# Kernel tuning notes

Measured on AMD Instinct MI355X. Metric: run time of the kernel, lower is better.

## Reference

```python
import jax, jax.numpy as jnp
import numpy as np

# Mamba2 config fixed by the wrapper: state=32, expand=1, n_groups=1, conv kernel=4
H, P, N, K = 32, 64, 32, 4          # heads, head_dim, state_size, conv kernel
D_MODEL = H * P                      # hidden = intermediate (expand=1) = 2048
CONV_DIM = D_MODEL + 2 * N           # intermediate + 2*n_groups*state = 2112
PROJ = D_MODEL + CONV_DIM + H        # in_proj width = 4192
EPS = 1e-6


def setup_inputs() -> dict:
    key = jax.random.key(0)
    ks = jax.random.split(key, 8)
    B, L = 4, 2048
    w = lambda k, shape, sc=0.02: jax.random.normal(k, shape, jnp.float32) * sc
    return {
        "x": jax.random.normal(ks[0], (B, L, D_MODEL), jnp.float32),
        "W_in": w(ks[1], (D_MODEL, PROJ)),
        "b_in": jnp.zeros((PROJ,), jnp.float32),
        "conv_w": w(ks[2], (CONV_DIM, K), 0.25),
        "conv_b": jnp.zeros((CONV_DIM,), jnp.float32),
        "A_log": jnp.log(jnp.arange(1, H + 1, dtype=jnp.float32)),
        "dt_bias": jax.random.uniform(ks[3], (H,), jnp.float32, -4.0, 0.0),
        "D_param": jnp.ones((H,), jnp.float32),
        "norm_w": jnp.ones((D_MODEL,), jnp.float32),
        "W_out": w(ks[4], (D_MODEL, D_MODEL)),
    }


def reference(x, W_in, b_in, conv_w, conv_b, A_log, dt_bias, D_param, norm_w, W_out):
    B, L, _ = x.shape
    proj = x @ W_in + b_in                                   # (B,L,PROJ)
    gate, hBC, dt_raw = jnp.split(proj, [D_MODEL, D_MODEL + CONV_DIM], axis=-1)

    # causal depthwise conv1d over time (kernel K, left pad K-1), then SiLU
    hp = jnp.pad(hBC, ((0, 0), (K - 1, 0), (0, 0)))
    conv = conv_b + sum(hp[:, k:k + L, :] * conv_w[:, k] for k in range(K))
    conv = jax.nn.silu(conv)

    xs, Bm, Cm = jnp.split(conv, [D_MODEL, D_MODEL + N], axis=-1)
    xs = xs.reshape(B, L, H, P)                              # (B,L,H,P)

    A = -jnp.exp(A_log)                                      # (H,)
    dt = jax.nn.softplus(dt_raw + dt_bias)                   # (B,L,H)
    dA = jnp.exp(dt * A)                                     # (B,L,H)

    def step(hstate, inp):
        dA_t, dt_t, x_t, B_t, C_t = inp                      # (B,H),(B,H),(B,H,P),(B,N),(B,N)
        upd = (dt_t[:, :, None] * x_t)[..., None] * B_t[:, None, None, :]
        hstate = dA_t[:, :, None, None] * hstate + upd       # (B,H,P,N)
        y_t = jnp.einsum('bhpn,bn->bhp', hstate, C_t)
        return hstate, y_t

    h0 = jnp.zeros((B, H, P, N), x.dtype)
    scan_in = (dA.transpose(1, 0, 2), dt.transpose(1, 0, 2),
               xs.transpose(1, 0, 2, 3), Bm.transpose(1, 0, 2), Cm.transpose(1, 0, 2))
    _, ys = jax.lax.scan(step, h0, scan_in)                  # ys: (L,B,H,P)

    y = ys.transpose(1, 0, 2, 3) + D_param[None, None, :, None] * xs
    y = y.reshape(B, L, D_MODEL)

    # gated RMSNorm: gate applied before normalization (MambaRMSNormGated)
    y = y * jax.nn.silu(gate)
    var = jnp.mean(jnp.square(y), axis=-1, keepdims=True)
    y = y * jax.lax.rsqrt(var + EPS) * norm_w
    return y @ W_out
```

## Files before the change

### kernel.cpp

```cpp
#include <hip/hip_runtime.h>
#include <cstdint>
#include <cstddef>

constexpr int kB    = 4;
constexpr int kL    = 2048;
constexpr int kH    = 32;
constexpr int kP    = 64;
constexpr int kN    = 32;
constexpr int kD    = 2048;
constexpr int kProjW = 4192;
constexpr int kLdp  = 4224;
constexpr int kM    = kB * kL;
constexpr int kK    = kD;
constexpr int kLC   = 64;
constexpr int kNC   = kL / kLC;

typedef _Float16 f16x8 __attribute__((ext_vector_type(8)));
typedef float f32x4 __attribute__((ext_vector_type(4)));

__device__ __forceinline__ float lane_bcast(float v, int lane) {
    return __int_as_float(__builtin_amdgcn_readlane(__float_as_int(v), lane));
}
__device__ __forceinline__ float silu_f(float x) { return x / (1.f + __expf(-x)); }

__device__ __forceinline__ void async_copy16(const void* g, void* lds) {
    __builtin_amdgcn_global_load_lds(
        (const __attribute__((address_space(1))) unsigned int*)(uintptr_t)g,
        (__attribute__((address_space(3))) unsigned int*)(uintptr_t)lds,
        16, 0, 0);
}

__global__ __launch_bounds__(256) void cast_f16_kernel(const float* __restrict__ in,
                                                       _Float16* __restrict__ out) {
    size_t i = ((size_t)blockIdx.x * 256 + threadIdx.x) * 8;
    float4 a = *(const float4*)(in + i);
    float4 b = *(const float4*)(in + i + 4);
    f16x8 o;
    o[0] = (_Float16)a.x; o[1] = (_Float16)a.y; o[2] = (_Float16)a.z; o[3] = (_Float16)a.w;
    o[4] = (_Float16)b.x; o[5] = (_Float16)b.y; o[6] = (_Float16)b.z; o[7] = (_Float16)b.w;
    *(f16x8*)(out + i) = o;
}

__global__ __launch_bounds__(256) void transpose_cast_kernel(const float* __restrict__ W,
                                                             _Float16* __restrict__ Wt,
                                                             int R, int C) {
    __shared__ float tile[32][33];
    const int c0 = blockIdx.x * 32;
    const int r0 = blockIdx.y * 32;
    const int tx = threadIdx.x & 31;
    const int ty = threadIdx.x >> 5;
    #pragma unroll
    for (int i = 0; i < 32; i += 8) {
        int rr = r0 + ty + i;
        int cc = c0 + tx;
        tile[ty + i][tx] = (cc < C) ? W[(size_t)rr * C + cc] : 0.f;
    }
    __syncthreads();
    #pragma unroll
    for (int i = 0; i < 32; i += 8) {
        int cc = c0 + ty + i;
        int rr = r0 + tx;
        Wt[(size_t)cc * R + rr] = (_Float16)tile[tx][ty + i];
    }
}

template <bool OUT_F16>
__global__ __launch_bounds__(512, 2) void gemm256_kernel(
    const _Float16* __restrict__ A, const _Float16* __restrict__ Bt,
    const float* __restrict__ bias, int nbias,
    void* __restrict__ Cout, int K, int ldc, int nvalid, int nn)
{
    __shared__ __attribute__((aligned(16))) _Float16 lds[2 * 4 * 8192];

    const int tid = threadIdx.x;
    const int l = tid & 63, r = l & 15, q = l >> 4;
    const int w = tid >> 6, wm = w >> 2, wn = w & 3;

    const int nwg = gridDim.x;
    const int q8 = nwg >> 3;
    const int pid = blockIdx.x;
    const int wg = (pid & 7) * q8 + (pid >> 3);
    const int m_idx = wg / nn;
    const int n_idx = wg - m_idx * nn;
    const size_t tileM = (size_t)m_idx * 256;
    const size_t tileN = (size_t)n_idx * 256;

    const int sR = ((tid >> 7) << 4) | (tid & 15);
    const int sC = ((tid >> 4) & 7) << 3;
    const _Float16* aSrc = A  + (tileM + sR) * (size_t)K + sC;
    const _Float16* bSrc = Bt + (tileN + sR) * (size_t)K + sC;
    _Float16* dst0 = lds + tid * 8;

    auto STAGE = [&](int buf, int part, const _Float16* src, int half, int kt2) {
        const _Float16* s = src + (size_t)(half * 128) * K + kt2 * 64;
        _Float16* d = dst0 + buf * 32768 + part * 8192;
        async_copy16(s, d);
        async_copy16(s + (size_t)64 * K, d + 4096);
    };

    const int NT = K >> 5 >> 1;
    STAGE(0, 0, aSrc, 0, 0); STAGE(0, 1, aSrc, 1, 0);
    STAGE(0, 2, bSrc, 0, 0); STAGE(0, 3, bSrc, 1, 0);
    STAGE(1, 0, aSrc, 0, 1); STAGE(1, 3, bSrc, 1, 1);
    asm volatile("s_waitcnt vmcnt(4)" ::: "memory");
    asm volatile("s_barrier" ::: "memory");

    f32x4 acc[8][4] = {};
    f16x8 afr[4][2], bfr[2][2], bfr2[2][2];

    const int aRd = wm * 4 * 2048 + l * 16;
    const int bRd = wn * 2 * 2048 + l * 16;

#define MFMA_CL(AO, BO, BARR, KK)                                                        \
    _Pragma("unroll")                                                                    \
    for (int i = 0; i < 4; ++i)                                                          \
        _Pragma("unroll")                                                                \
        for (int j = 0; j < 2; ++j)                                                      \
            acc[(AO) + i][(BO) + j] = __builtin_amdgcn_mfma_f32_16x16x32_f16(            \
                afr[i][KK], BARR[j][KK], acc[(AO) + i][(BO) + j], 0, 0, 0);

    for (int kt = 0; kt < NT; ++kt) {
        const int bsel = kt & 1;
        const char* a0p = (const char*)lds + bsel * 65536;
        const char* a1p = a0p + 16384;
        const char* b0p = a0p + 2 * 16384;
        const char* b1p = a0p + 3 * 16384;

        afr[0][0] = *(const f16x8*)(a0p + aRd);
        afr[1][0] = *(const f16x8*)(a0p + aRd + 2048);
        afr[2][0] = *(const f16x8*)(a0p + aRd + 4096);
        afr[3][0] = *(const f16x8*)(a0p + aRd + 6144);
        afr[0][1] = *(const f16x8*)(a0p + aRd + 1024);
        afr[1][1] = *(const f16x8*)(a0p + aRd + 3072);
        afr[2][1] = *(const f16x8*)(a0p + aRd + 5120);
        afr[3][1] = *(const f16x8*)(a0p + aRd + 7168);
        bfr[0][0] = *(const f16x8*)(b0p + bRd);
        bfr[1][0] = *(const f16x8*)(b0p + bRd + 2048);
        bfr[0][1] = *(const f16x8*)(b0p + bRd + 1024);
        bfr[1][1] = *(const f16x8*)(b0p + bRd + 3072);
        __builtin_amdgcn_sched_barrier(0);
        bfr2[0][0] = *(const f16x8*)(b1p + bRd);
        bfr2[1][0] = *(const f16x8*)(b1p + bRd + 2048);
        bfr2[0][1] = *(const f16x8*)(b1p + bRd + 1024);
        bfr2[1][1] = *(const f16x8*)(b1p + bRd + 3072);
        if (kt + 1 < NT) {
            STAGE(bsel ^ 1, 2, bSrc, 0, kt + 1);
            STAGE(bsel ^ 1, 1, aSrc, 1, kt + 1);
        }
        asm volatile("s_waitcnt lgkmcnt(4)" ::: "memory");
        __builtin_amdgcn_sched_barrier(0);
        __builtin_amdgcn_s_setprio(1);
        MFMA_CL(0, 0, bfr, 0)
        MFMA_CL(0, 0, bfr, 1)
        asm volatile("s_waitcnt lgkmcnt(0)" ::: "memory");
        __builtin_amdgcn_sched_barrier(0);
        MFMA_CL(0, 2, bfr2, 0)
        MFMA_CL(0, 2, bfr2, 1)
        __builtin_amdgcn_s_setprio(0);

        afr[0][0] = *(const f16x8*)(a1p + aRd);
        afr[1][0] = *(const f16x8*)(a1p + aRd + 2048);
        afr[2][0] = *(const f16x8*)(a1p + aRd + 4096);
        afr[3][0] = *(const f16x8*)(a1p + aRd + 6144);
        afr[0][1] = *(const f16x8*)(a1p + aRd + 1024);
        afr[1][1] = *(const f16x8*)(a1p + aRd + 3072);
        afr[2][1] = *(const f16x8*)(a1p + aRd + 5120);
        afr[3][1] = *(const f16x8*)(a1p + aRd + 7168);
        asm volatile("s_barrier" ::: "memory");
        if (kt + 2 < NT) {
            STAGE(bsel, 0, aSrc, 0, kt + 2);
            STAGE(bsel, 3, bSrc, 1, kt + 2);
        }
        asm volatile("s_waitcnt lgkmcnt(0)" ::: "memory");
        __builtin_amdgcn_sched_barrier(0);
        __builtin_amdgcn_s_setprio(1);
        MFMA_CL(4, 2, bfr2, 0)
        MFMA_CL(4, 2, bfr2, 1)
        MFMA_CL(4, 0, bfr, 0)
        MFMA_CL(4, 0, bfr, 1)
        __builtin_amdgcn_s_setprio(0);
        if (kt + 2 < NT) asm volatile("s_waitcnt vmcnt(4)" ::: "memory");
        else             asm volatile("s_waitcnt vmcnt(0)" ::: "memory");
        asm volatile("s_barrier" ::: "memory");
    }
#undef MFMA_CL

    #pragma unroll
    for (int bb = 0; bb < 4; ++bb) {
        const int nh = bb >> 1, j = bb & 1;
        const int col = (int)tileN + nh * 128 + wn * 32 + j * 16 + r;
        if (col >= nvalid) continue;
        float bv = 0.f;
        if (bias != nullptr && col < nbias) bv = bias[col];
        #pragma unroll
        for (int aa = 0; aa < 8; ++aa) {
            const int mh = aa >> 2, i = aa & 3;
            const size_t row = tileM + (size_t)(mh * 128 + wm * 64 + i * 16 + q * 4);
            #pragma unroll
            for (int u = 0; u < 4; ++u) {
                float v = acc[aa][bb][u] + bv;
                if (OUT_F16) ((_Float16*)Cout)[(row + u) * (size_t)ldc + col] = (_Float16)v;
                else         ((float*)Cout)[(row + u) * (size_t)ldc + col] = v;
            }
        }
    }
}

__global__ __launch_bounds__(256) void gemm_tail_kernel(
    const _Float16* __restrict__ A, const _Float16* __restrict__ Bt,
    const float* __restrict__ bias , _Float16* __restrict__ Cout,
    const float* __restrict__ A_log, const float* __restrict__ dt_bias,
    float* __restrict__ dtv, float* __restrict__ dAv)
{
    __shared__ __attribute__((aligned(16))) _Float16 lds[2 * 10240];
    const int K = kK;
    const int tid = threadIdx.x;
    const int l = tid & 63, r = l & 15, q = l >> 4;
    const int w = tid >> 6;
    const size_t tileM = (size_t)blockIdx.x * 32;

    const int sRa = ((tid >> 7) << 4) | (tid & 15);
    const int sC  = ((tid >> 4) & 7) << 3;
    const _Float16* aSrc = A + (tileM + sRa) * (size_t)K + sC;
    const _Float16* bSrc = Bt + (size_t)sRa * K + sC;
    _Float16* dst0 = lds + tid * 8;

    auto STG = [&](int buf, int kt2) {
        const _Float16* a = aSrc + kt2 * 64;
        const _Float16* b = bSrc + kt2 * 64;
        _Float16* d = dst0 + buf * 10240;
        async_copy16(a, d);
        #pragma unroll
        for (int c = 0; c < 4; ++c)
            async_copy16(b + (size_t)(c * 32) * K, d + 2048 + c * 2048);
    };

    const int NT = K / 64;
    STG(0, 0); STG(1, 1);
    asm volatile("s_waitcnt vmcnt(5)" ::: "memory");
    asm volatile("s_barrier" ::: "memory");

    f32x4 acc[2][2] = {};
    f16x8 af[2][2], bf[2][2];
    const int aRdT = l * 16;
    const int bRdT = 4096 + w * 2 * 2048 + l * 16;

    for (int kt = 0; kt < NT; ++kt) {
        const char* base = (const char*)lds + (kt & 1) * 20480;
        af[0][0] = *(const f16x8*)(base + aRdT);
        af[1][0] = *(const f16x8*)(base + aRdT + 2048);
        af[0][1] = *(const f16x8*)(base + aRdT + 1024);
        af[1][1] = *(const f16x8*)(base + aRdT + 3072);
        bf[0][0] = *(const f16x8*)(base + bRdT);
        bf[1][0] = *(const f16x8*)(base + bRdT + 2048);
        bf[0][1] = *(const f16x8*)(base + bRdT + 1024);
        bf[1][1] = *(const f16x8*)(base + bRdT + 3072);
        asm volatile("s_waitcnt lgkmcnt(0)" ::: "memory");
        __builtin_amdgcn_sched_barrier(0);
        asm volatile("s_barrier" ::: "memory");
        if (kt + 2 < NT) STG(kt & 1, kt + 2);
        #pragma unroll
        for (int kk = 0; kk < 2; ++kk)
            #pragma unroll
            for (int i = 0; i < 2; ++i)
                #pragma unroll
                for (int j = 0; j < 2; ++j)
                    acc[i][j] = __builtin_amdgcn_mfma_f32_16x16x32_f16(af[i][kk], bf[j][kk], acc[i][j], 0, 0, 0);
        if (kt + 2 < NT) asm volatile("s_waitcnt vmcnt(5)" ::: "memory");
        else             asm volatile("s_waitcnt vmcnt(0)" ::: "memory");
        asm volatile("s_barrier" ::: "memory");
    }

    #pragma unroll
    for (int j = 0; j < 2; ++j) {
        const int colOff = w * 32 + j * 16 + r;
        const float bv = (colOff < 96) ? bias[colOff] : 0.f;
        #pragma unroll
        for (int i = 0; i < 2; ++i) {
            #pragma unroll
            for (int u = 0; u < 4; ++u) {
                const size_t row = tileM + (size_t)(i * 16 + q * 4 + u);
                float v = acc[i][j][u] + bv;
                Cout[row * kLdp + 4096 + colOff] = (_Float16)v;
            }
        }
        if (colOff >= 64 && colOff < 96) {
            const int h = colOff - 64;
            const float db = dt_bias[h];
            const float nA = -expf(A_log[h]);
            #pragma unroll
            for (int i = 0; i < 2; ++i) {
                #pragma unroll
                for (int u = 0; u < 4; ++u) {
                    const size_t row = tileM + (size_t)(i * 16 + q * 4 + u);
                    const int b = (int)(row >> 11), t = (int)(row & 2047);
                    float z = acc[i][j][u] + bv + db;
                    float dt = (z > 20.f) ? z : log1pf(expf(z));
                    float dA = expf(dt * nA);
                    const size_t idx = (((size_t)b * kH + h) << 11) | t;
                    dtv[idx] = dt;
                    dAv[idx] = dA;
                }
            }
        }
    }
}

__global__ __launch_bounds__(64) void scan_pass1_kernel(
    const _Float16* __restrict__ projh, const float* __restrict__ conv_w,
    const float* __restrict__ conv_b, const float* __restrict__ dtv,
    const float* __restrict__ dAv, float* __restrict__ cstate, float* __restrict__ Pch)
{
    const int blk = blockIdx.x;
    const int c   = blk & (kNC - 1);
    const int bh  = blk >> 5;
    const int h   = bh & (kH - 1);
    const int b   = bh >> 5;
    const int l   = threadIdx.x;
    const int t0  = c * kLC;

    const int chx = h * kP + l;
    const int chb = 2048 + (l & 31);
    const float xw0 = conv_w[chx*4+0], xw1 = conv_w[chx*4+1], xw2 = conv_w[chx*4+2], xw3 = conv_w[chx*4+3];
    const float xbb = conv_b[chx];
    const float bw0 = conv_w[chb*4+0], bw1 = conv_w[chb*4+1], bw2 = conv_w[chb*4+2], bw3 = conv_w[chb*4+3];
    const float bbb = conv_b[chb];

    const _Float16* pb = projh + (size_t)b * kL * kLdp;
    const int colx = 2048 + chx;
    const int colb = 2048 + chb;

    float xq0=0.f, xq1=0.f, xq2=0.f, bq0=0.f, bq1=0.f, bq2=0.f;
    if (c > 0) {
        xq0 = (float)pb[(size_t)(t0-3)*kLdp + colx];
        xq1 = (float)pb[(size_t)(t0-2)*kLdp + colx];
        xq2 = (float)pb[(size_t)(t0-1)*kLdp + colx];
        bq0 = (float)pb[(size_t)(t0-3)*kLdp + colb];
        bq1 = (float)pb[(size_t)(t0-2)*kLdp + colb];
        bq2 = (float)pb[(size_t)(t0-1)*kLdp + colb];
    }

    float hs[kN];
    #pragma unroll
    for (int n = 0; n < kN; ++n) hs[n] = 0.f;
    float Pp = 1.f;
    const float* dtp = dtv + (size_t)bh * kL;
    const float* dAp = dAv + (size_t)bh * kL;

    float xv = (float)pb[(size_t)t0 * kLdp + colx];
    float bv = (float)pb[(size_t)t0 * kLdp + colb];
    float dt = dtp[t0], dA = dAp[t0];

    #pragma unroll 1
    for (int t = t0; t < t0 + kLC; ++t) {
        float xn = 0.f, bn = 0.f, dtn = 0.f, dAn = 0.f;
        if (t + 1 < t0 + kLC) {
            const size_t ro2 = (size_t)(t + 1) * kLdp;
            xn = (float)pb[ro2 + colx];
            bn = (float)pb[ro2 + colb];
            dtn = dtp[t + 1]; dAn = dAp[t + 1];
        }
        float sx = silu_f(xbb + xw0*xq0 + xw1*xq1 + xw2*xq2 + xw3*xv);
        float sb = silu_f(bbb + bw0*bq0 + bw1*bq1 + bw2*bq2 + bw3*bv);
        xq0=xq1; xq1=xq2; xq2=xv;
        bq0=bq1; bq1=bq2; bq2=bv;
        float dtx = dt * sx;
        Pp *= dA;
        #pragma unroll
        for (int n = 0; n < kN; ++n)
            hs[n] = fmaf(dA, hs[n], dtx * lane_bcast(sb, n));
        xv = xn; bv = bn; dt = dtn; dA = dAn;
    }
    float* cs = cstate + (size_t)blk * (kP * kN) + l * kN;
    #pragma unroll
    for (int n = 0; n < kN; ++n) cs[n] = hs[n];
    if (l == 0) Pch[blk] = Pp;
}

__global__ __launch_bounds__(256) void scan_pass2_kernel(float* __restrict__ cstate,
                                                         const float* __restrict__ Pch) {
    const int bh  = blockIdx.x;
    const int off = threadIdx.x * 8;
    float s[8];
    #pragma unroll
    for (int i = 0; i < 8; ++i) s[i] = 0.f;
    float* base = cstate + (size_t)bh * (kNC * kP * kN) + off;
    #pragma unroll 1
    for (int c = 0; c < kNC; ++c) {
        float* cs = base + c * (kP * kN);
        float Pp = Pch[bh * kNC + c];
        #pragma unroll
        for (int i = 0; i < 8; ++i) {
            float loc = cs[i];
            cs[i] = s[i];
            s[i] = fmaf(Pp, s[i], loc);
        }
    }
}

__global__ __launch_bounds__(64) void scan_pass3_kernel(
    const _Float16* __restrict__ projh, const float* __restrict__ conv_w,
    const float* __restrict__ conv_b, const float* __restrict__ dtv,
    const float* __restrict__ dAv, const float* __restrict__ cstate,
    const float* __restrict__ D_param, float* __restrict__ ypre)
{
    const int blk = blockIdx.x;
    const int c   = blk & (kNC - 1);
    const int bh  = blk >> 5;
    const int h   = bh & (kH - 1);
    const int b   = bh >> 5;
    const int l   = threadIdx.x;
    const int t0  = c * kLC;

    const int chx = h * kP + l;
    const int chc = 2048 + l;
    const float xw0 = conv_w[chx*4+0], xw1 = conv_w[chx*4+1], xw2 = conv_w[chx*4+2], xw3 = conv_w[chx*4+3];
    const float xbb = conv_b[chx];
    const float cw0 = conv_w[chc*4+0], cw1 = conv_w[chc*4+1], cw2 = conv_w[chc*4+2], cw3 = conv_w[chc*4+3];
    const float cbb = conv_b[chc];

    const _Float16* pb = projh + (size_t)b * kL * kLdp;
    const int colx = 2048 + chx;
    const int colc = 2048 + chc;

    float xq0=0.f, xq1=0.f, xq2=0.f, cq0=0.f, cq1=0.f, cq2=0.f;
    if (c > 0) {
        xq0 = (float)pb[(size_t)(t0-3)*kLdp + colx];
        xq1 = (float)pb[(size_t)(t0-2)*kLdp + colx];
        xq2 = (float)pb[(size_t)(t0-1)*kLdp + colx];
        cq0 = (float)pb[(size_t)(t0-3)*kLdp + colc];
        cq1 = (float)pb[(size_t)(t0-2)*kLdp + colc];
        cq2 = (float)pb[(size_t)(t0-1)*kLdp + colc];
    }

    float hs[kN];
    const float* cs = cstate + (size_t)blk * (kP * kN) + l * kN;
    #pragma unroll
    for (int n = 0; n < kN; ++n) hs[n] = cs[n];
    const float Dh = D_param[h];
    const float* dtp = dtv + (size_t)bh * kL;
    const float* dAp = dAv + (size_t)bh * kL;
    float* yo = ypre + (size_t)b * kL * kD + h * kP + l;

    float xv = (float)pb[(size_t)t0 * kLdp + colx];
    float cv = (float)pb[(size_t)t0 * kLdp + colc];
    float dt = dtp[t0], dA = dAp[t0];

    #pragma unroll 1
    for (int t = t0; t < t0 + kLC; ++t) {
        float xn = 0.f, cn2 = 0.f, dtn = 0.f, dAn = 0.f;
        if (t + 1 < t0 + kLC) {
            const size_t ro2 = (size_t)(t + 1) * kLdp;
            xn = (float)pb[ro2 + colx];
            cn2 = (float)pb[ro2 + colc];
            dtn = dtp[t + 1]; dAn = dAp[t + 1];
        }
        float sx = silu_f(xbb + xw0*xq0 + xw1*xq1 + xw2*xq2 + xw3*xv);
        float sc = silu_f(cbb + cw0*cq0 + cw1*cq1 + cw2*cq2 + cw3*cv);
        xq0=xq1; xq1=xq2; xq2=xv;
        cq0=cq1; cq1=cq2; cq2=cv;
        float dtx = dt * sx;
        float y0 = Dh * sx, y1 = 0.f;
        #pragma unroll
        for (int n = 0; n < kN; ++n) {
            float bn = lane_bcast(sc, n);
            float cn = lane_bcast(sc, n + 32);
            hs[n] = fmaf(dA, hs[n], dtx * bn);
            if (n & 1) y1 = fmaf(hs[n], cn, y1);
            else       y0 = fmaf(hs[n], cn, y0);
        }
        yo[(size_t)t * kD] = y0 + y1;
        xv = xn; cv = cn2; dt = dtn; dA = dAn;
    }
}

__global__ __launch_bounds__(256) void gated_norm_kernel(
    const float* __restrict__ ypre, const _Float16* __restrict__ projh,
    const float* __restrict__ norm_w, _Float16* __restrict__ yh)
{
    const int row = blockIdx.x;
    const int tid = threadIdx.x;
    const float* yr = ypre + (size_t)row * kD;
    const _Float16* gr = projh + (size_t)row * kLdp;
    float v[8];
    float ss = 0.f;
    #pragma unroll
    for (int u = 0; u < 8; ++u) {
        int col = tid + u * 256;
        float g = (float)gr[col];
        float t = yr[col] * (g / (1.f + __expf(-g)));
        v[u] = t;
        ss = fmaf(t, t, ss);
    }
    #pragma unroll
    for (int off = 32; off > 0; off >>= 1) ss += __shfl_xor(ss, off, 64);
    __shared__ float red[4];
    if ((tid & 63) == 0) red[tid >> 6] = ss;
    __syncthreads();
    float tot = (red[0] + red[1]) + (red[2] + red[3]);
    float scl = rsqrtf(tot * (1.f / (float)kD) + 1e-6f);
    #pragma unroll
    for (int u = 0; u < 8; ++u) {
        int col = tid + u * 256;
        yh[(size_t)row * kD + col] = (_Float16)(v[u] * scl * norm_w[col]);
    }
}

extern "C" void kernel_launch(void* const* d_in, const int* in_sizes, int n_in,
                              void* d_out, int out_size, void* d_ws, size_t ws_size,
                              hipStream_t stream)
{
    (void)in_sizes; (void)n_in; (void)out_size; (void)ws_size;
    const float* x       = (const float*)d_in[0];
    const float* W_in    = (const float*)d_in[1];
    const float* b_in    = (const float*)d_in[2];
    const float* conv_w  = (const float*)d_in[3];
    const float* conv_b  = (const float*)d_in[4];
    const float* A_log   = (const float*)d_in[5];
    const float* dt_bias = (const float*)d_in[6];
    const float* D_param = (const float*)d_in[7];
    const float* norm_w  = (const float*)d_in[8];
    const float* W_out   = (const float*)d_in[9];
    float* out = (float*)d_out;

    char* p = (char*)d_ws;
    _Float16* projh = (_Float16*)p; p += (size_t)kM * kLdp * 2;
    _Float16* xh    = (_Float16*)p; p += (size_t)kM * kD * 2;
    _Float16* Wt    = (_Float16*)p; p += (size_t)kLdp * kK * 2;
    _Float16* Wot   = (_Float16*)p; p += (size_t)kD * kK * 2;
    float* dtv      = (float*)p;    p += (size_t)kB * kH * kL * 4;
    float* dAv      = (float*)p;    p += (size_t)kB * kH * kL * 4;
    float* Pch      = (float*)p;    p += (size_t)kB * kH * kNC * 4;
    float* cstate = (float*)xh;
    _Float16* yh  = xh;
    float* ypre = out;

    cast_f16_kernel<<<(kM * kD) / (256 * 8), 256, 0, stream>>>(x, xh);
    transpose_cast_kernel<<<dim3(kLdp / 32, kK / 32), 256, 0, stream>>>(W_in, Wt, kK, kProjW);
    transpose_cast_kernel<<<dim3(kD / 32, kK / 32), 256, 0, stream>>>(W_out, Wot, kK, kD);
    gemm256_kernel<true><<<512, 512, 0, stream>>>(
        xh, Wt, b_in, kProjW, (void*)projh, kK, kLdp, 4096, 16);
    gemm_tail_kernel<<<kM / 32, 256, 0, stream>>>(
        xh, Wt + (size_t)4096 * kK, b_in + 4096, projh, A_log, dt_bias, dtv, dAv);
    scan_pass1_kernel<<<kB * kH * kNC, 64, 0, stream>>>(projh, conv_w, conv_b, dtv, dAv, cstate, Pch);
    scan_pass2_kernel<<<kB * kH, 256, 0, stream>>>(cstate, Pch);
    scan_pass3_kernel<<<kB * kH * kNC, 64, 0, stream>>>(projh, conv_w, conv_b, dtv, dAv, cstate, D_param, ypre);
    gated_norm_kernel<<<kM, 256, 0, stream>>>(ypre, projh, norm_w, yh);
    gemm256_kernel<false><<<256, 512, 0, stream>>>(
        yh, Wot, nullptr, 0, (void*)out, kK, kD, kD, 8);
}
```

Baseline: 620.2 us.

## Simplify GEMM double-buffer pipeline and stagger LDS quadrant order across wave groups

Replaces the split half-tile prefetch (two stages issued at different points with a mid-iteration barrier) with a plain double buffer that prefetches the whole next K-tile at loop top and waits vmcnt(0) once per iteration. Odd wave groups read the A/B quadrants in the opposite order from even groups, which is meant to spread LDS bank and port pressure and drops the intra-iteration barrier. The cost is less overlap between global loads and compute, because each iteration now waits for all outstanding loads before it can continue.

```diff
diff --git a/kernel.cpp b/kernel.cpp
--- a/kernel.cpp
+++ b/kernel.cpp
@@ -98,11 +98,10 @@
         async_copy16(s + (size_t)64 * K, d + 4096);
     };
 
-    const int NT = K >> 5 >> 1;
+    const int NT = K >> 6;
     STAGE(0, 0, aSrc, 0, 0); STAGE(0, 1, aSrc, 1, 0);
     STAGE(0, 2, bSrc, 0, 0); STAGE(0, 3, bSrc, 1, 0);
-    STAGE(1, 0, aSrc, 0, 1); STAGE(1, 3, bSrc, 1, 1);
-    asm volatile("s_waitcnt vmcnt(4)" ::: "memory");
+    asm volatile("s_waitcnt vmcnt(0)" ::: "memory");
     asm volatile("s_barrier" ::: "memory");
 
     f32x4 acc[8][4] = {};
@@ -119,71 +118,90 @@
             acc[(AO) + i][(BO) + j] = __builtin_amdgcn_mfma_f32_16x16x32_f16(            \
                 afr[i][KK], BARR[j][KK], acc[(AO) + i][(BO) + j], 0, 0, 0);
 
-    for (int kt = 0; kt < NT; ++kt) {
-        const int bsel = kt & 1;
-        const char* a0p = (const char*)lds + bsel * 65536;
-        const char* a1p = a0p + 16384;
-        const char* b0p = a0p + 2 * 16384;
-        const char* b1p = a0p + 3 * 16384;
-
-        afr[0][0] = *(const f16x8*)(a0p + aRd);
-        afr[1][0] = *(const f16x8*)(a0p + aRd + 2048);
-        afr[2][0] = *(const f16x8*)(a0p + aRd + 4096);
-        afr[3][0] = *(const f16x8*)(a0p + aRd + 6144);
-        afr[0][1] = *(const f16x8*)(a0p + aRd + 1024);
-        afr[1][1] = *(const f16x8*)(a0p + aRd + 3072);
-        afr[2][1] = *(const f16x8*)(a0p + aRd + 5120);
-        afr[3][1] = *(const f16x8*)(a0p + aRd + 7168);
-        bfr[0][0] = *(const f16x8*)(b0p + bRd);
-        bfr[1][0] = *(const f16x8*)(b0p + bRd + 2048);
-        bfr[0][1] = *(const f16x8*)(b0p + bRd + 1024);
-        bfr[1][1] = *(const f16x8*)(b0p + bRd + 3072);
-        __builtin_amdgcn_sched_barrier(0);
-        bfr2[0][0] = *(const f16x8*)(b1p + bRd);
-        bfr2[1][0] = *(const f16x8*)(b1p + bRd + 2048);
-        bfr2[0][1] = *(const f16x8*)(b1p + bRd + 1024);
-        bfr2[1][1] = *(const f16x8*)(b1p + bRd + 3072);
-        if (kt + 1 < NT) {
-            STAGE(bsel ^ 1, 2, bSrc, 0, kt + 1);
-            STAGE(bsel ^ 1, 1, aSrc, 1, kt + 1);
-        }
-        asm volatile("s_waitcnt lgkmcnt(4)" ::: "memory");
-        __builtin_amdgcn_sched_barrier(0);
-        __builtin_amdgcn_s_setprio(1);
-        MFMA_CL(0, 0, bfr, 0)
-        MFMA_CL(0, 0, bfr, 1)
-        asm volatile("s_waitcnt lgkmcnt(0)" ::: "memory");
-        __builtin_amdgcn_sched_barrier(0);
-        MFMA_CL(0, 2, bfr2, 0)
-        MFMA_CL(0, 2, bfr2, 1)
-        __builtin_amdgcn_s_setprio(0);
-
-        afr[0][0] = *(const f16x8*)(a1p + aRd);
-        afr[1][0] = *(const f16x8*)(a1p + aRd + 2048);
-        afr[2][0] = *(const f16x8*)(a1p + aRd + 4096);
-        afr[3][0] = *(const f16x8*)(a1p + aRd + 6144);
-        afr[0][1] = *(const f16x8*)(a1p + aRd + 1024);
-        afr[1][1] = *(const f16x8*)(a1p + aRd + 3072);
-        afr[2][1] = *(const f16x8*)(a1p + aRd + 5120);
-        afr[3][1] = *(const f16x8*)(a1p + aRd + 7168);
-        asm volatile("s_barrier" ::: "memory");
-        if (kt + 2 < NT) {
-            STAGE(bsel, 0, aSrc, 0, kt + 2);
-            STAGE(bsel, 3, bSrc, 1, kt + 2);
-        }
-        asm volatile("s_waitcnt lgkmcnt(0)" ::: "memory");
-        __builtin_amdgcn_sched_barrier(0);
-        __builtin_amdgcn_s_setprio(1);
-        MFMA_CL(4, 2, bfr2, 0)
-        MFMA_CL(4, 2, bfr2, 1)
-        MFMA_CL(4, 0, bfr, 0)
-        MFMA_CL(4, 0, bfr, 1)
-        __builtin_amdgcn_s_setprio(0);
-        if (kt + 2 < NT) asm volatile("s_waitcnt vmcnt(4)" ::: "memory");
-        else             asm volatile("s_waitcnt vmcnt(0)" ::: "memory");
-        asm volatile("s_barrier" ::: "memory");
+#define RD_A(PBASE)                                                                      \
+    afr[0][0] = *(const f16x8*)((PBASE) + aRd);                                          \
+    afr[1][0] = *(const f16x8*)((PBASE) + aRd + 2048);                                   \
+    afr[2][0] = *(const f16x8*)((PBASE) + aRd + 4096);                                   \
+    afr[3][0] = *(const f16x8*)((PBASE) + aRd + 6144);                                   \
+    afr[0][1] = *(const f16x8*)((PBASE) + aRd + 1024);                                   \
+    afr[1][1] = *(const f16x8*)((PBASE) + aRd + 3072);                                   \
+    afr[2][1] = *(const f16x8*)((PBASE) + aRd + 5120);                                   \
+    afr[3][1] = *(const f16x8*)((PBASE) + aRd + 7168);
+
+#define RD_B(DST, PBASE)                                                                 \
+    DST[0][0] = *(const f16x8*)((PBASE) + bRd);                                          \
+    DST[1][0] = *(const f16x8*)((PBASE) + bRd + 2048);                                   \
+    DST[0][1] = *(const f16x8*)((PBASE) + bRd + 1024);                                   \
+    DST[1][1] = *(const f16x8*)((PBASE) + bRd + 3072);
+
+#define TILE_BODY(PAF, PBF, PBS, PAS, AOF, BOF, AOS, BOS)                                \
+    RD_A(PAF)                                                                            \
+    RD_B(bfr, PBF)                                                                       \
+    __builtin_amdgcn_sched_barrier(0);                                                   \
+    RD_B(bfr2, PBS)                                                                      \
+    __builtin_amdgcn_sched_barrier(0);                                                   \
+    asm volatile("s_waitcnt lgkmcnt(4)" ::: "memory");                                   \
+    __builtin_amdgcn_sched_barrier(0);                                                   \
+    __builtin_amdgcn_s_setprio(1);                                                       \
+    MFMA_CL(AOF, BOF, bfr, 0)                                                            \
+    MFMA_CL(AOF, BOF, bfr, 1)                                                            \
+    asm volatile("s_waitcnt lgkmcnt(0)" ::: "memory");                                   \
+    __builtin_amdgcn_sched_barrier(0);                                                   \
+    MFMA_CL(AOF, BOS, bfr2, 0)                                                           \
+    MFMA_CL(AOF, BOS, bfr2, 1)                                                           \
+    __builtin_amdgcn_s_setprio(0);                                                       \
+    RD_A(PAS)                                                                            \
+    __builtin_amdgcn_sched_barrier(0);                                                   \
+    asm volatile("s_waitcnt lgkmcnt(0)" ::: "memory");                                   \
+    __builtin_amdgcn_sched_barrier(0);                                                   \
+    __builtin_amdgcn_s_setprio(1);                                                       \
+    MFMA_CL(AOS, BOS, bfr2, 0)                                                           \
+    MFMA_CL(AOS, BOS, bfr2, 1)                                                           \
+    MFMA_CL(AOS, BOF, bfr, 0)                                                            \
+    MFMA_CL(AOS, BOF, bfr, 1)                                                            \
+    __builtin_amdgcn_s_setprio(0);
+
+#define TILE_STAGE_AND_SYNC                                                              \
+    if (kt + 1 < NT) {                                                                   \
+        STAGE(bsel ^ 1, 0, aSrc, 0, kt + 1);                                             \
+        STAGE(bsel ^ 1, 1, aSrc, 1, kt + 1);                                             \
+        STAGE(bsel ^ 1, 2, bSrc, 0, kt + 1);                                             \
+        STAGE(bsel ^ 1, 3, bSrc, 1, kt + 1);                                             \
+    }
+
+    const bool oddgrp = ((w >> 2) & 1) != 0;
+    if (!oddgrp) {
+        #pragma unroll 2
+        for (int kt = 0; kt < NT; ++kt) {
+            const int bsel = kt & 1;
+            const char* a0p = (const char*)lds + bsel * 65536;
+            const char* a1p = a0p + 16384;
+            const char* b0p = a0p + 2 * 16384;
+            const char* b1p = a0p + 3 * 16384;
+            TILE_STAGE_AND_SYNC
+            TILE_BODY(a0p, b0p, b1p, a1p, 0, 0, 4, 2)
+            asm volatile("s_waitcnt vmcnt(0)" ::: "memory");
+            asm volatile("s_barrier" ::: "memory");
+        }
+    } else {
+        #pragma unroll 2
+        for (int kt = 0; kt < NT; ++kt) {
+            const int bsel = kt & 1;
+            const char* a0p = (const char*)lds + bsel * 65536;
+            const char* a1p = a0p + 16384;
+            const char* b0p = a0p + 2 * 16384;
+            const char* b1p = a0p + 3 * 16384;
+            TILE_STAGE_AND_SYNC
+            TILE_BODY(a1p, b1p, b0p, a0p, 4, 2, 0, 0)
+            asm volatile("s_waitcnt vmcnt(0)" ::: "memory");
+            asm volatile("s_barrier" ::: "memory");
+        }
     }
 #undef MFMA_CL
+#undef RD_A
+#undef RD_B
+#undef TILE_BODY
+#undef TILE_STAGE_AND_SYNC
 
     #pragma unroll
     for (int bb = 0; bb < 4; ++bb) {
```

After: 649.3 us. +4.7%, slower.

## Replace 256x256 GEMM with 128x256 tile, 3-stage LDS pipeline

Applied to the files above, without the earlier changes.

Rewrites the main GEMM kernel to use 128x256 output tiles per 256-thread workgroup with a k-step of 32 and a triple-buffered LDS ring in place of the 256x256, 512-thread, double-buffered layout with split A/B halves. Each wave now computes a 64x128 sub-tile with one set of fragment loads per iteration, and both GEMM launches double their grid size. The aim is more workgroups for better CU occupancy and deeper prefetch. The cost is lower arithmetic intensity per tile, more global and LDS traffic, and a loop schedule that interleaves LDS reads with MFMA less finely. The nbias/nvalid guards are removed.

```diff
diff --git a/kernel.cpp b/kernel.cpp
--- a/kernel.cpp
+++ b/kernel.cpp
@@ -65,16 +65,16 @@
 }
 
 template <bool OUT_F16>
-__global__ __launch_bounds__(512, 2) void gemm256_kernel(
+__global__ __launch_bounds__(256, 2) void gemm128_kernel(
     const _Float16* __restrict__ A, const _Float16* __restrict__ Bt,
-    const float* __restrict__ bias, int nbias,
-    void* __restrict__ Cout, int K, int ldc, int nvalid, int nn)
+    const float* __restrict__ bias,
+    void* __restrict__ Cout, int K, int ldc, int nn)
 {
-    __shared__ __attribute__((aligned(16))) _Float16 lds[2 * 4 * 8192];
+    __shared__ __attribute__((aligned(16))) _Float16 lds[3 * 12288];
 
     const int tid = threadIdx.x;
     const int l = tid & 63, r = l & 15, q = l >> 4;
-    const int w = tid >> 6, wm = w >> 2, wn = w & 3;
+    const int w = tid >> 6, wm = w >> 1, wn = w & 1;
 
     const int nwg = gridDim.x;
     const int q8 = nwg >> 3;
@@ -82,123 +82,76 @@
     const int wg = (pid & 7) * q8 + (pid >> 3);
     const int m_idx = wg / nn;
     const int n_idx = wg - m_idx * nn;
-    const size_t tileM = (size_t)m_idx * 256;
+    const size_t tileM = (size_t)m_idx * 128;
     const size_t tileN = (size_t)n_idx * 256;
 
-    const int sR = ((tid >> 7) << 4) | (tid & 15);
-    const int sC = ((tid >> 4) & 7) << 3;
+    const int sR = ((tid >> 6) << 4) | (tid & 15);
+    const int sC = ((tid >> 4) & 3) << 3;
     const _Float16* aSrc = A  + (tileM + sR) * (size_t)K + sC;
     const _Float16* bSrc = Bt + (tileN + sR) * (size_t)K + sC;
     _Float16* dst0 = lds + tid * 8;
 
-    auto STAGE = [&](int buf, int part, const _Float16* src, int half, int kt2) {
-        const _Float16* s = src + (size_t)(half * 128) * K + kt2 * 64;
-        _Float16* d = dst0 + buf * 32768 + part * 8192;
-        async_copy16(s, d);
-        async_copy16(s + (size_t)64 * K, d + 4096);
+    auto STAGE = [&](int buf, int kt2) {
+        const _Float16* a = aSrc + kt2 * 32;
+        const _Float16* b = bSrc + kt2 * 32;
+        _Float16* d = dst0 + buf * 12288;
+        async_copy16(a, d);
+        async_copy16(a + (size_t)64 * K, d + 2048);
+        #pragma unroll
+        for (int c = 0; c < 4; ++c)
+            async_copy16(b + (size_t)(c * 64) * K, d + 4096 + c * 2048);
     };
 
-    const int NT = K >> 5 >> 1;
-    STAGE(0, 0, aSrc, 0, 0); STAGE(0, 1, aSrc, 1, 0);
-    STAGE(0, 2, bSrc, 0, 0); STAGE(0, 3, bSrc, 1, 0);
-    STAGE(1, 0, aSrc, 0, 1); STAGE(1, 3, bSrc, 1, 1);
-    asm volatile("s_waitcnt vmcnt(4)" ::: "memory");
+    const int NT = K >> 5;
+    STAGE(0, 0); STAGE(1, 1);
+    asm volatile("s_waitcnt vmcnt(6)" ::: "memory");
     asm volatile("s_barrier" ::: "memory");
 
-    f32x4 acc[8][4] = {};
-    f16x8 afr[4][2], bfr[2][2], bfr2[2][2];
-
-    const int aRd = wm * 4 * 2048 + l * 16;
-    const int bRd = wn * 2 * 2048 + l * 16;
-
-#define MFMA_CL(AO, BO, BARR, KK)                                                        \
-    _Pragma("unroll")                                                                    \
-    for (int i = 0; i < 4; ++i)                                                          \
-        _Pragma("unroll")                                                                \
-        for (int j = 0; j < 2; ++j)                                                      \
-            acc[(AO) + i][(BO) + j] = __builtin_amdgcn_mfma_f32_16x16x32_f16(            \
-                afr[i][KK], BARR[j][KK], acc[(AO) + i][(BO) + j], 0, 0, 0);
-
+    f32x4 acc[4][8] = {};
+    f16x8 af[4], bf[8];
+
+    const int aRd = wm * 4096 + l * 16;
+    const int bRd = 8192 + wn * 8192 + l * 16;
+
+    int cs = 0;
     for (int kt = 0; kt < NT; ++kt) {
-        const int bsel = kt & 1;
-        const char* a0p = (const char*)lds + bsel * 65536;
-        const char* a1p = a0p + 16384;
-        const char* b0p = a0p + 2 * 16384;
-        const char* b1p = a0p + 3 * 16384;
-
-        afr[0][0] = *(const f16x8*)(a0p + aRd);
-        afr[1][0] = *(const f16x8*)(a0p + aRd + 2048);
-        afr[2][0] = *(const f16x8*)(a0p + aRd + 4096);
-        afr[3][0] = *(const f16x8*)(a0p + aRd + 6144);
-        afr[0][1] = *(const f16x8*)(a0p + aRd + 1024);
-        afr[1][1] = *(const f16x8*)(a0p + aRd + 3072);
-        afr[2][1] = *(const f16x8*)(a0p + aRd + 5120);
-        afr[3][1] = *(const f16x8*)(a0p + aRd + 7168);
-        bfr[0][0] = *(const f16x8*)(b0p + bRd);
-        bfr[1][0] = *(const f16x8*)(b0p + bRd + 2048);
-        bfr[0][1] = *(const f16x8*)(b0p + bRd + 1024);
-        bfr[1][1] = *(const f16x8*)(b0p + bRd + 3072);
-        __builtin_amdgcn_sched_barrier(0);
-        bfr2[0][0] = *(const f16x8*)(b1p + bRd);
-        bfr2[1][0] = *(const f16x8*)(b1p + bRd + 2048);
-        bfr2[0][1] = *(const f16x8*)(b1p + bRd + 1024);
-        bfr2[1][1] = *(const f16x8*)(b1p + bRd + 3072);
-        if (kt + 1 < NT) {
-            STAGE(bsel ^ 1, 2, bSrc, 0, kt + 1);
-            STAGE(bsel ^ 1, 1, aSrc, 1, kt + 1);
-        }
-        asm volatile("s_waitcnt lgkmcnt(4)" ::: "memory");
-        __builtin_amdgcn_sched_barrier(0);
-        __builtin_amdgcn_s_setprio(1);
-        MFMA_CL(0, 0, bfr, 0)
-        MFMA_CL(0, 0, bfr, 1)
-        asm volatile("s_waitcnt lgkmcnt(0)" ::: "memory");
-        __builtin_amdgcn_sched_barrier(0);
-        MFMA_CL(0, 2, bfr2, 0)
-        MFMA_CL(0, 2, bfr2, 1)
-        __builtin_amdgcn_s_setprio(0);
-
-        afr[0][0] = *(const f16x8*)(a1p + aRd);
-        afr[1][0] = *(const f16x8*)(a1p + aRd + 2048);
-        afr[2][0] = *(const f16x8*)(a1p + aRd + 4096);
-        afr[3][0] = *(const f16x8*)(a1p + aRd + 6144);
-        afr[0][1] = *(const f16x8*)(a1p + aRd + 1024);
-        afr[1][1] = *(const f16x8*)(a1p + aRd + 3072);
-        afr[2][1] = *(const f16x8*)(a1p + aRd + 5120);
-        afr[3][1] = *(const f16x8*)(a1p + aRd + 7168);
-        asm volatile("s_barrier" ::: "memory");
+        const char* base = (const char*)lds + cs * 24576;
         if (kt + 2 < NT) {
-            STAGE(bsel, 0, aSrc, 0, kt + 2);
-            STAGE(bsel, 3, bSrc, 1, kt + 2);
-        }
+            int ns = cs + 2; if (ns >= 3) ns -= 3;
+            STAGE(ns, kt + 2);
+        }
+        #pragma unroll
+        for (int i = 0; i < 4; ++i)
+            af[i] = *(const f16x8*)(base + aRd + i * 1024);
+        #pragma unroll
+        for (int j = 0; j < 8; ++j)
+            bf[j] = *(const f16x8*)(base + bRd + j * 1024);
         asm volatile("s_waitcnt lgkmcnt(0)" ::: "memory");
         __builtin_amdgcn_sched_barrier(0);
         __builtin_amdgcn_s_setprio(1);
-        MFMA_CL(4, 2, bfr2, 0)
-        MFMA_CL(4, 2, bfr2, 1)
-        MFMA_CL(4, 0, bfr, 0)
-        MFMA_CL(4, 0, bfr, 1)
+        #pragma unroll
+        for (int i = 0; i < 4; ++i)
+            #pragma unroll
+            for (int j = 0; j < 8; ++j)
+                acc[i][j] = __builtin_amdgcn_mfma_f32_16x16x32_f16(af[i], bf[j], acc[i][j], 0, 0, 0);
         __builtin_amdgcn_s_setprio(0);
-        if (kt + 2 < NT) asm volatile("s_waitcnt vmcnt(4)" ::: "memory");
+        if (kt + 2 < NT) asm volatile("s_waitcnt vmcnt(6)" ::: "memory");
         else             asm volatile("s_waitcnt vmcnt(0)" ::: "memory");
         asm volatile("s_barrier" ::: "memory");
-    }
-#undef MFMA_CL
-
-    #pragma unroll
-    for (int bb = 0; bb < 4; ++bb) {
-        const int nh = bb >> 1, j = bb & 1;
-        const int col = (int)tileN + nh * 128 + wn * 32 + j * 16 + r;
-        if (col >= nvalid) continue;
+        cs = (cs + 1 >= 3) ? 0 : cs + 1;
+    }
+
+    #pragma unroll
+    for (int j = 0; j < 8; ++j) {
+        const int col = (int)tileN + wn * 128 + j * 16 + r;
         float bv = 0.f;
-        if (bias != nullptr && col < nbias) bv = bias[col];
-        #pragma unroll
-        for (int aa = 0; aa < 8; ++aa) {
-            const int mh = aa >> 2, i = aa & 3;
-            const size_t row = tileM + (size_t)(mh * 128 + wm * 64 + i * 16 + q * 4);
+        if (bias != nullptr) bv = bias[col];
+        #pragma unroll
+        for (int i = 0; i < 4; ++i) {
+            const size_t row = tileM + (size_t)(wm * 64 + i * 16 + q * 4);
             #pragma unroll
             for (int u = 0; u < 4; ++u) {
-                float v = acc[aa][bb][u] + bv;
+                float v = acc[i][j][u] + bv;
                 if (OUT_F16) ((_Float16*)Cout)[(row + u) * (size_t)ldc + col] = (_Float16)v;
                 else         ((float*)Cout)[(row + u) * (size_t)ldc + col] = v;
             }
@@ -538,14 +491,14 @@
     cast_f16_kernel<<<(kM * kD) / (256 * 8), 256, 0, stream>>>(x, xh);
     transpose_cast_kernel<<<dim3(kLdp / 32, kK / 32), 256, 0, stream>>>(W_in, Wt, kK, kProjW);
     transpose_cast_kernel<<<dim3(kD / 32, kK / 32), 256, 0, stream>>>(W_out, Wot, kK, kD);
-    gemm256_kernel<true><<<512, 512, 0, stream>>>(
-        xh, Wt, b_in, kProjW, (void*)projh, kK, kLdp, 4096, 16);
+    gemm128_kernel<true><<<1024, 256, 0, stream>>>(
+        xh, Wt, b_in, (void*)projh, kK, kLdp, 16);
     gemm_tail_kernel<<<kM / 32, 256, 0, stream>>>(
         xh, Wt + (size_t)4096 * kK, b_in + 4096, projh, A_log, dt_bias, dtv, dAv);
     scan_pass1_kernel<<<kB * kH * kNC, 64, 0, stream>>>(projh, conv_w, conv_b, dtv, dAv, cstate, Pch);
     scan_pass2_kernel<<<kB * kH, 256, 0, stream>>>(cstate, Pch);
     scan_pass3_kernel<<<kB * kH * kNC, 64, 0, stream>>>(projh, conv_w, conv_b, dtv, dAv, cstate, D_param, ypre);
     gated_norm_kernel<<<kM, 256, 0, stream>>>(ypre, projh, norm_w, yh);
-    gemm256_kernel<false><<<256, 512, 0, stream>>>(
-        yh, Wot, nullptr, 0, (void*)out, kK, kD, kD, 8);
-}
+    gemm128_kernel<false><<<512, 256, 0, stream>>>(
+        yh, Wot, nullptr, (void*)out, kK, kD, 8);
+}
```

Measured after the change: 694.3 us. 11.9% more time.
